# Kernel tuning notes

Measured on AMD Instinct MI355X. Metric: run time of the kernel, lower is better.

Reference implementation:

```python
import jax, jax.numpy as jnp
import numpy as np

B, N = 4096, 12
HID = 64
SLOPE = 0.2   # GATv2Conv default negative_slope
ALPHA = 0.1   # skip-connection scale


def _gabriel_adjacency(p):
    # p: [B, N, 2] node positions. Gabriel graph: edge (i,j) iff no other
    # point k lies inside the closed disk with diameter segment (p_i, p_j).
    n = p.shape[1]
    mid = (p[:, :, None, :] + p[:, None, :, :]) * 0.5                      # [B,N,N,2]
    r2 = jnp.sum((p[:, :, None, :] - p[:, None, :, :]) ** 2, -1) * 0.25    # [B,N,N]
    d2 = jnp.sum((p[:, None, None, :, :] - mid[:, :, :, None, :]) ** 2, -1)  # [B,i,j,k]
    eye = jnp.eye(n, dtype=bool)
    excl = eye[:, None, :] | eye[None, :, :]                               # k==i or k==j
    d2 = jnp.where(excl[None], jnp.inf, d2)
    gab = jnp.all(d2 > r2[..., None], axis=-1) & (~eye)[None]
    # undirected edges + self loops (GATv2Conv add_self_loops=True default)
    return gab | jnp.swapaxes(gab, 1, 2) | eye[None]                       # [B,N,N]


def _gatv2(x, adj, wl, wr, att, b):
    # PyG GATv2Conv, heads=1: e_ij = att . leaky_relu(W_l x_j + W_r x_i),
    # alpha = softmax_j(e_ij) over neighbors, out_i = sum_j alpha_ij W_l x_j + b.
    xl = x @ wl                                                            # source feats [B,N,H]
    xr = x @ wr                                                            # target feats [B,N,H]
    s = jax.nn.leaky_relu(xl[:, None, :, :] + xr[:, :, None, :], SLOPE)    # [B,i,j,H]
    e = jnp.einsum('bijh,h->bij', s, att)
    e = jnp.where(adj, e, -1e9)
    a = jax.nn.softmax(e, axis=-1)                                         # over sources j
    return jnp.einsum('bij,bjh->bih', a, xl) + b


def _forward(batch, enc_w1, enc_b1, enc_w2, enc_b2, enc_w3, enc_b3,
             g1_wl, g1_wr, g1_att, g1_b, g2_wl, g2_wr, g2_att, g2_b,
             g3_wl, g3_wr, g3_att, g3_b, g4_wl, g4_wr, g4_att, g4_b,
             lab_w, lab_b, val_w, val_b, skip_w, skip_b):
    h = jax.nn.relu(batch @ enc_w1 + enc_b1)
    h = jax.nn.relu(h @ enc_w2 + enc_b2)
    latent = h @ enc_w3 + enc_b3                                           # [B,N,3]
    # graph construction is non-differentiable (scipy in the original)
    adj = _gabriel_adjacency(jax.lax.stop_gradient(latent[..., :2]))
    x0 = latent[..., 2:3]                                                  # [B,N,1]
    x1 = jax.nn.relu(_gatv2(x0, adj, g1_wl, g1_wr, g1_att, g1_b))
    x2 = jax.nn.relu(_gatv2(x1, adj, g2_wl, g2_wr, g2_att, g2_b))
    skip = latent @ skip_w + skip_b
    x3 = jax.nn.relu(_gatv2(x2, adj, g3_wl, g3_wr, g3_att, g3_b) + ALPHA * skip)
    logits = x3 @ lab_w + lab_b                                            # [B,N,4]
    # note: original feeds x2 (not x3) into gcn4 -- kept faithful
    x4 = jax.nn.relu(_gatv2(x2, adj, g4_wl, g4_wr, g4_att, g4_b) + ALPHA * skip)
    values = x4 @ val_w + val_b                                            # [B,N,1]
    return batch[:, :, :4], batch[:, :, 4:5], logits, values, latent


def setup_inputs():
    key = jax.random.key(0)
    ks = iter(jax.random.split(key, 40))
    def rnd(shape, s=0.1):
        return jax.random.normal(next(ks), shape, dtype=jnp.float32) * s
    inp = {"batch": jax.random.normal(next(ks), (B, N, 5), dtype=jnp.float32)}
    inp.update(enc_w1=rnd((5, HID)), enc_b1=jnp.zeros((HID,), jnp.float32),
               enc_w2=rnd((HID, HID)), enc_b2=jnp.zeros((HID,), jnp.float32),
               enc_w3=rnd((HID, 3)), enc_b3=jnp.zeros((3,), jnp.float32))
    for i, cin in zip((1, 2, 3, 4), (1, HID, HID, HID)):
        inp[f"g{i}_wl"] = rnd((cin, HID)); inp[f"g{i}_wr"] = rnd((cin, HID))
        inp[f"g{i}_att"] = rnd((HID,)); inp[f"g{i}_b"] = jnp.zeros((HID,), jnp.float32)
    inp.update(lab_w=rnd((HID, 4)), lab_b=jnp.zeros((4,), jnp.float32),
               val_w=rnd((HID, 1)), val_b=jnp.zeros((1,), jnp.float32),
               skip_w=rnd((3, HID)), skip_b=jnp.zeros((HID,), jnp.float32))
    return inp


def reference(batch, enc_w1, enc_b1, enc_w2, enc_b2, enc_w3, enc_b3,
              g1_wl, g1_wr, g1_att, g1_b, g2_wl, g2_wr, g2_att, g2_b,
              g3_wl, g3_wr, g3_att, g3_b, g4_wl, g4_wr, g4_att, g4_b,
              lab_w, lab_b, val_w, val_b, skip_w, skip_b):
    return _forward(batch, enc_w1, enc_b1, enc_w2, enc_b2, enc_w3, enc_b3,
                    g1_wl, g1_wr, g1_att, g1_b, g2_wl, g2_wr, g2_att, g2_b,
                    g3_wl, g3_wr, g3_att, g3_b, g4_wl, g4_wr, g4_att, g4_b,
                    lab_w, lab_b, val_w, val_b, skip_w, skip_b)
```

## Files before the change

### kernel.cpp

```cpp
#include <hip/hip_runtime.h>
#include <hip/hip_bf16.h>
#include <math.h>

#define N     12
#define HID   64
#define STP   68
#define XST   72
#define SLOPE 0.2f
#define ALPHA 0.1f

typedef float v2f __attribute__((ext_vector_type(2)));
typedef float v4f __attribute__((ext_vector_type(4)));
typedef int   i4  __attribute__((ext_vector_type(4)));
typedef short v8s __attribute__((ext_vector_type(8)));

static __device__ __forceinline__ v8s as_v8s(i4 v) {
    union { i4 a; v8s b; } u; u.a = v; return u.b;
}
static __device__ __forceinline__ unsigned short f2bf(float f) {
    __hip_bfloat16 h = __float2bfloat16(f);
    return *(unsigned short*)&h;
}
static __device__ __forceinline__ float bf2f(unsigned short u) {
    return __uint_as_float((unsigned)u << 16);
}

#define OUT0 0
#define OUT1 196608
#define OUT2 245760
#define OUT3 442368
#define OUT4 491520

__global__ void prep_kernel(const float* __restrict__ enc_w2,
                            const float* __restrict__ g2_wl, const float* __restrict__ g2_wr,
                            const float* __restrict__ g3_wl, const float* __restrict__ g3_wr,
                            const float* __restrict__ g4_wl, const float* __restrict__ g4_wr,
                            const float* __restrict__ lab_w,
                            float* __restrict__ ws) {
    int t = threadIdx.x;
    int bx = blockIdx.x;
    if (bx < 64) { ws[t*64 + bx] = enc_w2[bx*64 + t]; return; }
    if (bx == 112) {
        #pragma unroll
        for (int c = 0; c < 4; c++) ws[16384 + c*64 + t] = lab_w[t*4 + c];
        return;
    }
    int idx = bx - 64;
    int mat = idx >> 3, rem = idx & 7;
    int kt = rem >> 2, nt = rem & 3;
    const float* src;
    switch (mat) {
        case 0: src = g2_wl; break;
        case 1: src = g2_wr; break;
        case 2: src = g3_wl; break;
        case 3: src = g3_wr; break;
        case 4: src = g4_wl; break;
        default: src = g4_wr; break;
    }
    int quad = t >> 4, col = t & 15;
    int n = nt*16 + col;
    unsigned* dst = (unsigned*)(ws + 4096) + mat*2048 + (kt*4+nt)*256 + t*4;
    #pragma unroll
    for (int jp = 0; jp < 4; jp++) {
        int k0 = kt*32 + quad*8 + 2*jp;
        dst[jp] = (unsigned)f2bf(src[(k0+0)*64 + n]) | ((unsigned)f2bf(src[(k0+1)*64 + n]) << 16);
    }
}

template<bool TW>
__global__ __launch_bounds__(64, 3) void gae_kernel(
    const float* __restrict__ batch,
    const float* __restrict__ enc_w1, const float* __restrict__ enc_b1,
    const float* __restrict__ enc_w2, const float* __restrict__ enc_b2,
    const float* __restrict__ enc_w3, const float* __restrict__ enc_b3,
    const float* __restrict__ g1_wl, const float* __restrict__ g1_wr,
    const float* __restrict__ g1_att, const float* __restrict__ g1_b,
    const float* __restrict__ g2_wl, const float* __restrict__ g2_wr,
    const float* __restrict__ g2_att, const float* __restrict__ g2_b,
    const float* __restrict__ g3_wl, const float* __restrict__ g3_wr,
    const float* __restrict__ g3_att, const float* __restrict__ g3_b,
    const float* __restrict__ g4_wl, const float* __restrict__ g4_wr,
    const float* __restrict__ g4_att, const float* __restrict__ g4_b,
    const float* __restrict__ lab_w, const float* __restrict__ lab_b,
    const float* __restrict__ val_w, const float* __restrict__ val_b,
    const float* __restrict__ skip_w, const float* __restrict__ skip_b,
    const float* __restrict__ wsT,
    float* __restrict__ out)
{
    const int b = blockIdx.x;
    const int t = threadIdx.x;

    __shared__ __align__(16) unsigned char smem[7424];
    float* h1 = (float*)smem;
    float* h2 = (float*)(smem + 3264);
    unsigned short* xl16 = (unsigned short*)smem;
    unsigned short* xr16 = (unsigned short*)(smem + 1728);
    unsigned short* xB16 = (unsigned short*)(smem + 3456);
    float* pool  = (float*)(smem + 6528);
    float* att_s = (float*)(smem + 7104);
    unsigned char* pairs8 = smem + 7360;

    const v2f z2 = {0.f, 0.f};
    const v4f z4 = {0.f, 0.f, 0.f, 0.f};
    const v2f sl2 = {SLOPE, SLOPE};

    const int p0 = t,        i0 = p0 / N, j0 = p0 - i0*N;
    const int p1 = t + 64,   i1 = p1 / N, j1 = p1 - i1*N;
    const int p2 = (t < 16) ? (t + 128) : 143;
    const int i2 = p2 / N,   j2 = p2 - i2*N;

    if (t < N*5) {
        float v = batch[b*(N*5) + t];
        int i = t / 5, f = t - i*5;
        if (f < 4) out[OUT0 + (size_t)b*(N*4) + i*4 + f] = v;
        else       out[OUT1 + (size_t)b*N + i] = v;
    }

    {
        float acc[N];
        float bias = enc_b1[t];
        #pragma unroll
        for (int i=0;i<N;i++) acc[i] = bias;
        const float* brow = batch + b*(N*5);
        #pragma unroll
        for (int f=0; f<5; f++) {
            float w = enc_w1[f*HID + t];
            #pragma unroll
            for (int i=0;i<N;i++) acc[i] = fmaf(brow[i*5+f], w, acc[i]);
        }
        #pragma unroll
        for (int i=0;i<N;i++) h1[i*STP + t] = fmaxf(acc[i], 0.f);
    }
    __syncthreads();

    {
        v2f acc[N];
        #pragma unroll
        for (int i=0;i<N;i++) acc[i] = z2;
        const float* w2p = TW ? (wsT + t*HID) : nullptr;
        for (int c=0;c<HID;c+=4) {
            v2f w01, w23;
            if (TW) {
                v4f w4 = *reinterpret_cast<const v4f*>(&w2p[c]);
                w01 = w4.xy; w23 = w4.zw;
            } else {
                w01 = (v2f){enc_w2[(c+0)*HID+t], enc_w2[(c+1)*HID+t]};
                w23 = (v2f){enc_w2[(c+2)*HID+t], enc_w2[(c+3)*HID+t]};
            }
            #pragma unroll
            for (int i=0;i<N;i++) {
                v4f xv = *reinterpret_cast<const v4f*>(&h1[i*STP + c]);
                acc[i] = __builtin_elementwise_fma(xv.xy, w01, acc[i]);
                acc[i] = __builtin_elementwise_fma(xv.zw, w23, acc[i]);
            }
        }
        float bias = enc_b2[t];
        #pragma unroll
        for (int i=0;i<N;i++) h2[i*STP + t] = fmaxf(bias + acc[i].x + acc[i].y, 0.f);
    }
    __syncthreads();

    if (t < N*3) {
        int i = t / 3, c = t - i*3;
        float acc = enc_b3[c];
        for (int k=0;k<HID;k+=4) {
            v4f xv = *reinterpret_cast<const v4f*>(&h2[i*STP + k]);
            acc = fmaf(xv.x, enc_w3[(k+0)*3+c], acc);
            acc = fmaf(xv.y, enc_w3[(k+1)*3+c], acc);
            acc = fmaf(xv.z, enc_w3[(k+2)*3+c], acc);
            acc = fmaf(xv.w, enc_w3[(k+3)*3+c], acc);
        }
        pool[t] = acc;
        out[OUT4 + (size_t)b*(N*3) + t] = acc;
    }
    __syncthreads();

    float kx[N], ky[N], kz[N];
    #pragma unroll
    for (int k=0;k<N;k++) { kx[k]=pool[k*3]; ky[k]=pool[k*3+1]; kz[k]=pool[k*3+2]; }

    float skipv[N];
    {
        float w0 = skip_w[t], w1 = skip_w[HID+t], w2 = skip_w[2*HID+t];
        float bias = skip_b[t];
        #pragma unroll
        for (int i=0;i<N;i++)
            skipv[i] = fmaf(kx[i], w0, fmaf(ky[i], w1, fmaf(kz[i], w2, bias)));
    }

    auto gab = [&](int i, int j)->bool {
        if (i == j) return false;
        float pix = pool[i*3], piy = pool[i*3+1];
        float pjx = pool[j*3], pjy = pool[j*3+1];
        float mx = (pix + pjx) * 0.5f, my = (piy + pjy) * 0.5f;
        float dx = pix - pjx, dy = piy - pjy;
        float r2 = (dx*dx + dy*dy) * 0.25f;
        bool g = true;
        #pragma unroll
        for (int k=0;k<N;k++) {
            float ex = kx[k] - mx, ey = ky[k] - my;
            bool ok = (k == i) || (k == j) || (ex*ex + ey*ey > r2);
            g = g && ok;
        }
        return g;
    };
    unsigned long long gb0 = __ballot(gab(i0, j0));
    unsigned long long gb1 = __ballot(gab(i1, j1));
    unsigned long long gb2 = __ballot((t < 16) && gab(i2, j2));
    auto gbit = [&](int p)->int {
        unsigned long long m = (p < 64) ? gb0 : ((p < 128) ? gb1 : gb2);
        return (int)((m >> (p & 63)) & 1ull);
    };
    const int adjA = gbit(p0) | gbit(j0*N+i0) | (i0 == j0);
    const int adjB = gbit(p1) | gbit(j1*N+i1) | (i1 == j1);
    const int adjC = (t < 16) ? (gbit(p2) | gbit(j2*N+i2) | (i2 == j2)) : 0;

    auto mbcnt64 = [&](unsigned long long m)->int {
        return __builtin_amdgcn_mbcnt_hi((unsigned)(m >> 32),
               __builtin_amdgcn_mbcnt_lo((unsigned)m, 0));
    };
    const unsigned long long am0 = __ballot(adjA != 0);
    const unsigned long long am1 = __ballot(adjB != 0);
    const unsigned long long am2 = __ballot(adjC != 0);
    const int c0  = __popcll(am0);
    const int c01 = c0 + __popcll(am1);
    const int nv  = c01 + __popcll(am2);
    const int idx0 = mbcnt64(am0);
    const int idx1 = c0  + mbcnt64(am1);
    const int idx2 = c01 + mbcnt64(am2);
    if (adjA)               pairs8[idx0] = (unsigned char)p0;
    if (adjB && idx1 < 64)  pairs8[idx1] = (unsigned char)p1;
    if (adjC && idx2 < 64)  pairs8[idx2] = (unsigned char)p2;
    const bool ovB = adjB && (idx1 >= 64);
    const bool ovC = adjC && (idx2 >= 64);
    const int nvc = nv < 64 ? nv : 64;

    auto scoreAt = [&](int i, int j)->float {
        const unsigned* Lj = (const unsigned*)&xl16[j*XST];
        const unsigned* Ri = (const unsigned*)&xr16[i*XST];
        v2f a2 = z2;
        for (int h=0; h<HID; h+=8) {
            i4 lw = *reinterpret_cast<const i4*>(Lj + (h>>1));
            i4 rw = *reinterpret_cast<const i4*>(Ri + (h>>1));
            v4f aa = *reinterpret_cast<const v4f*>(&att_s[h]);
            v4f ab = *reinterpret_cast<const v4f*>(&att_s[h+4]);
            #pragma unroll
            for (int q=0; q<4; q++) {
                unsigned lu = (unsigned)lw[q], ru = (unsigned)rw[q];
                v2f xl2 = { __uint_as_float(lu << 16), __uint_as_float(lu & 0xffff0000u) };
                v2f xr2 = { __uint_as_float(ru << 16), __uint_as_float(ru & 0xffff0000u) };
                v2f s = xl2 + xr2;
                v2f l = __builtin_elementwise_fma(sl2, __builtin_elementwise_min(s, z2),
                                                  __builtin_elementwise_max(s, z2));
                v2f av = (q==0) ? aa.xy : (q==1) ? aa.zw : (q==2) ? ab.xy : ab.zw;
                a2 = __builtin_elementwise_fma(av, l, a2);
            }
        }
        return a2.x + a2.y;
    };

    auto gat_core = [&](const float* __restrict__ att, const float* __restrict__ gb,
                        unsigned short* __restrict__ out16, int useSkip) {
        att_s[t] = att[t];
        pool[t] = 0.f; pool[t+64] = 0.f;
        if (t < 16) pool[t+128] = 0.f;
        __syncthreads();
        if (t < nvc) {
            int p = pairs8[t];
            int i = (p * 171) >> 11;
            int j = p - i*N;
            pool[p] = __expf(scoreAt(i, j));
        }
        if (nv > 64) {
            if (ovB) pool[p1] = __expf(scoreAt(i1, j1));
            if (ovC) pool[p2] = __expf(scoreAt(i2, j2));
        }
        __syncthreads();
        {
            float xj[N];
            #pragma unroll
            for (int j=0;j<N;j++) xj[j] = bf2f(xl16[j*XST + t]);
            v4f X0 = {xj[0], xj[1], xj[2],  xj[3]};
            v4f X1 = {xj[4], xj[5], xj[6],  xj[7]};
            v4f X2 = {xj[8], xj[9], xj[10], xj[11]};
            float bias = gb[t];
            #pragma unroll
            for (int i=0;i<N;i++) {
                const v4f* ep = reinterpret_cast<const v4f*>(&pool[i*N]);
                v4f e0 = ep[0], e1 = ep[1], e2 = ep[2];
                float sum = ((e0.x+e0.y)+(e0.z+e0.w))
                          + ((e1.x+e1.y)+(e1.z+e1.w))
                          + ((e2.x+e2.y)+(e2.z+e2.w));
                v4f acc = __builtin_elementwise_fma(e0, X0,
                          __builtin_elementwise_fma(e1, X1, e2*X2));
                float r = bias + ((acc.x + acc.y) + (acc.z + acc.w)) / sum;
                if (useSkip) r = fmaf(ALPHA, skipv[i], r);
                out16[i*XST + t] = f2bf(fmaxf(r, 0.f));
            }
        }
        __syncthreads();
    };

    auto stage_mfma = [&](int matL) {
        const int m = t & 15, quad = t >> 4;
        const int mc = (m < N) ? m : 0;
        i4 aF0 = *reinterpret_cast<const i4*>(&xB16[mc*XST + quad*8]);
        i4 aF1 = *reinterpret_cast<const i4*>(&xB16[mc*XST + 32 + quad*8]);
        const i4* bbase = reinterpret_cast<const i4*>(wsT + 4096);
        #pragma unroll
        for (int mm=0; mm<2; mm++) {
            const i4* bp = bbase + (matL + mm)*512;
            v4f acc[4] = {z4, z4, z4, z4};
            #pragma unroll
            for (int nt=0; nt<4; nt++) {
                i4 b0 = bp[(0*4+nt)*64 + t];
                i4 b1 = bp[(1*4+nt)*64 + t];
                acc[nt] = __builtin_amdgcn_mfma_f32_16x16x32_bf16(as_v8s(aF0), as_v8s(b0), acc[nt], 0, 0, 0);
                acc[nt] = __builtin_amdgcn_mfma_f32_16x16x32_bf16(as_v8s(aF1), as_v8s(b1), acc[nt], 0, 0, 0);
            }
            unsigned short* dst = (mm == 0) ? xl16 : xr16;
            if (quad < 3) {
                #pragma unroll
                for (int nt=0; nt<4; nt++) {
                    #pragma unroll
                    for (int r=0; r<4; r++)
                        dst[(quad*4+r)*XST + nt*16 + m] = f2bf(acc[nt][r]);
                }
            }
        }
    };

    auto stage = [&](const float* __restrict__ wl, const float* __restrict__ wr) {
        v2f al[N], ar[N];
        #pragma unroll
        for (int i=0;i<N;i++) { al[i] = z2; ar[i] = z2; }
        for (int c=0;c<HID;c+=2) {
            v2f wlv = (v2f){wl[(c+0)*HID+t], wl[(c+1)*HID+t]};
            v2f wrv = (v2f){wr[(c+0)*HID+t], wr[(c+1)*HID+t]};
            #pragma unroll
            for (int i=0;i<N;i++) {
                unsigned xu = *(const unsigned*)&xB16[i*XST + c];
                v2f xv = { __uint_as_float(xu << 16), __uint_as_float(xu & 0xffff0000u) };
                al[i] = __builtin_elementwise_fma(xv, wlv, al[i]);
                ar[i] = __builtin_elementwise_fma(xv, wrv, ar[i]);
            }
        }
        #pragma unroll
        for (int i=0;i<N;i++) {
            xl16[i*XST + t] = f2bf(al[i].x + al[i].y);
            xr16[i*XST + t] = f2bf(ar[i].x + ar[i].y);
        }
    };

    {
        float wlv = g1_wl[t], wrv = g1_wr[t];
        #pragma unroll
        for (int i=0;i<N;i++) {
            xl16[i*XST + t] = f2bf(kz[i] * wlv);
            xr16[i*XST + t] = f2bf(kz[i] * wrv);
        }
    }
    gat_core(g1_att, g1_b, xB16, 0);

    if (TW) stage_mfma(0); else stage(g2_wl, g2_wr);
    gat_core(g2_att, g2_b, xB16, 0);

    if (TW) stage_mfma(2); else stage(g3_wl, g3_wr);
    gat_core(g3_att, g3_b, xr16, 1);

    if (t < N*4) {
        int i = t >> 2, c = t & 3;
        float acc = lab_b[c];
        const unsigned* xp = (const unsigned*)&xr16[i*XST];
        if (TW) {
            const float* lwT = wsT + 16384 + c*HID;
            for (int h=0;h<HID;h+=2) {
                unsigned xu = xp[h>>1];
                acc = fmaf(__uint_as_float(xu << 16), lwT[h], acc);
                acc = fmaf(__uint_as_float(xu & 0xffff0000u), lwT[h+1], acc);
            }
        } else {
            for (int h=0;h<HID;h+=2) {
                unsigned xu = xp[h>>1];
                acc = fmaf(__uint_as_float(xu << 16), lab_w[(h+0)*4+c], acc);
                acc = fmaf(__uint_as_float(xu & 0xffff0000u), lab_w[(h+1)*4+c], acc);
            }
        }
        out[OUT2 + (size_t)b*(N*4) + t] = acc;
    }

    if (TW) stage_mfma(4); else stage(g4_wl, g4_wr);
    gat_core(g4_att, g4_b, xr16, 1);

    if (t < N) {
        float acc = val_b[0];
        const unsigned* xp = (const unsigned*)&xr16[t*XST];
        for (int h=0;h<HID;h+=2) {
            unsigned xu = xp[h>>1];
            acc = fmaf(__uint_as_float(xu << 16), val_w[h], acc);
            acc = fmaf(__uint_as_float(xu & 0xffff0000u), val_w[h+1], acc);
        }
        out[OUT3 + (size_t)b*N + t] = acc;
    }
}

extern "C" void kernel_launch(void* const* d_in, const int* in_sizes, int n_in,
                              void* d_out, int out_size, void* d_ws, size_t ws_size,
                              hipStream_t stream) {
    (void)in_sizes; (void)n_in; (void)out_size;
    const bool useT = (ws_size >= (16384 + 256)*sizeof(float));
    if (useT) {
        prep_kernel<<<dim3(113), dim3(64), 0, stream>>>(
            (const float*)d_in[3],
            (const float*)d_in[11], (const float*)d_in[12],
            (const float*)d_in[15], (const float*)d_in[16],
            (const float*)d_in[19], (const float*)d_in[20],
            (const float*)d_in[23],
            (float*)d_ws);
        gae_kernel<true><<<dim3(4096), dim3(64), 0, stream>>>(
            (const float*)d_in[0],
            (const float*)d_in[1],  (const float*)d_in[2],
            (const float*)d_in[3],  (const float*)d_in[4],
            (const float*)d_in[5],  (const float*)d_in[6],
            (const float*)d_in[7],  (const float*)d_in[8],  (const float*)d_in[9],  (const float*)d_in[10],
            (const float*)d_in[11], (const float*)d_in[12], (const float*)d_in[13], (const float*)d_in[14],
            (const float*)d_in[15], (const float*)d_in[16], (const float*)d_in[17], (const float*)d_in[18],
            (const float*)d_in[19], (const float*)d_in[20], (const float*)d_in[21], (const float*)d_in[22],
            (const float*)d_in[23], (const float*)d_in[24],
            (const float*)d_in[25], (const float*)d_in[26],
            (const float*)d_in[27], (const float*)d_in[28],
            (const float*)d_ws,
            (float*)d_out);
    } else {
        gae_kernel<false><<<dim3(4096), dim3(64), 0, stream>>>(
            (const float*)d_in[0],
            (const float*)d_in[1],  (const float*)d_in[2],
            (const float*)d_in[3],  (const float*)d_in[4],
            (const float*)d_in[5],  (const float*)d_in[6],
            (const float*)d_in[7],  (const float*)d_in[8],  (const float*)d_in[9],  (const float*)d_in[10],
            (const float*)d_in[11], (const float*)d_in[12], (const float*)d_in[13], (const float*)d_in[14],
            (const float*)d_in[15], (const float*)d_in[16], (const float*)d_in[17], (const float*)d_in[18],
            (const float*)d_in[19], (const float*)d_in[20], (const float*)d_in[21], (const float*)d_in[22],
            (const float*)d_in[23], (const float*)d_in[24],
            (const float*)d_in[25], (const float*)d_in[26],
            (const float*)d_in[27], (const float*)d_in[28],
            nullptr,
            (float*)d_out);
    }
}
```

Baseline: 174.5 us.

## Reduce register pressure: read pool from LDS, split shared buffers, batch Gabriel tests

Drops the per-thread kx/ky/kz register arrays and reads latent coordinates from shared memory instead. The batch row is now staged through LDS for the first encoder layer. The three Gabriel pair tests per thread are interleaved in one loop over k. Shared memory becomes separate named arrays instead of one aliased byte buffer, and an extra barrier is added before stage 4. The aim is lower VGPR use and better latency hiding, at the cost of more LDS reads, extra barriers and a larger LDS footprint.

Result: no change. 176.7 us (+1.3%).

```diff
diff --git a/kernel.cpp b/kernel.cpp
--- a/kernel.cpp
+++ b/kernel.cpp
@@ -90,15 +90,15 @@
     const int b = blockIdx.x;
     const int t = threadIdx.x;
 
-    __shared__ __align__(16) unsigned char smem[7424];
-    float* h1 = (float*)smem;
-    float* h2 = (float*)(smem + 3264);
-    unsigned short* xl16 = (unsigned short*)smem;
-    unsigned short* xr16 = (unsigned short*)(smem + 1728);
-    unsigned short* xB16 = (unsigned short*)(smem + 3456);
-    float* pool  = (float*)(smem + 6528);
-    float* att_s = (float*)(smem + 7104);
-    unsigned char* pairs8 = smem + 7360;
+    __shared__ __align__(16) float bufA[N*STP];
+    __shared__ __align__(16) float bufB[N*STP];
+    __shared__ __align__(16) unsigned short xB16[N*XST];
+    __shared__ __align__(16) float pool[144];
+    __shared__ __align__(16) float att_s[HID];
+    __shared__ __align__(16) unsigned char pairs8[64];
+
+    unsigned short* xl16 = (unsigned short*)bufA;
+    unsigned short* xr16 = (unsigned short*)bufB;
 
     const v2f z2 = {0.f, 0.f};
     const v4f z4 = {0.f, 0.f, 0.f, 0.f};
@@ -111,25 +111,26 @@
 
     if (t < N*5) {
         float v = batch[b*(N*5) + t];
+        pool[t] = v;
         int i = t / 5, f = t - i*5;
         if (f < 4) out[OUT0 + (size_t)b*(N*4) + i*4 + f] = v;
         else       out[OUT1 + (size_t)b*N + i] = v;
     }
+    __syncthreads();
 
     {
         float acc[N];
         float bias = enc_b1[t];
         #pragma unroll
         for (int i=0;i<N;i++) acc[i] = bias;
-        const float* brow = batch + b*(N*5);
         #pragma unroll
         for (int f=0; f<5; f++) {
             float w = enc_w1[f*HID + t];
             #pragma unroll
-            for (int i=0;i<N;i++) acc[i] = fmaf(brow[i*5+f], w, acc[i]);
-        }
-        #pragma unroll
-        for (int i=0;i<N;i++) h1[i*STP + t] = fmaxf(acc[i], 0.f);
+            for (int i=0;i<N;i++) acc[i] = fmaf(pool[i*5+f], w, acc[i]);
+        }
+        #pragma unroll
+        for (int i=0;i<N;i++) bufA[i*STP + t] = fmaxf(acc[i], 0.f);
     }
     __syncthreads();
 
@@ -149,14 +150,14 @@
             }
             #pragma unroll
             for (int i=0;i<N;i++) {
-                v4f xv = *reinterpret_cast<const v4f*>(&h1[i*STP + c]);
+                v4f xv = *reinterpret_cast<const v4f*>(&bufA[i*STP + c]);
                 acc[i] = __builtin_elementwise_fma(xv.xy, w01, acc[i]);
                 acc[i] = __builtin_elementwise_fma(xv.zw, w23, acc[i]);
             }
         }
         float bias = enc_b2[t];
         #pragma unroll
-        for (int i=0;i<N;i++) h2[i*STP + t] = fmaxf(bias + acc[i].x + acc[i].y, 0.f);
+        for (int i=0;i<N;i++) bufB[i*STP + t] = fmaxf(bias + acc[i].x + acc[i].y, 0.f);
     }
     __syncthreads();
 
@@ -164,7 +165,7 @@
         int i = t / 3, c = t - i*3;
         float acc = enc_b3[c];
         for (int k=0;k<HID;k+=4) {
-            v4f xv = *reinterpret_cast<const v4f*>(&h2[i*STP + k]);
+            v4f xv = *reinterpret_cast<const v4f*>(&bufB[i*STP + k]);
             acc = fmaf(xv.x, enc_w3[(k+0)*3+c], acc);
             acc = fmaf(xv.y, enc_w3[(k+1)*3+c], acc);
             acc = fmaf(xv.z, enc_w3[(k+2)*3+c], acc);
@@ -175,38 +176,52 @@
     }
     __syncthreads();
 
-    float kx[N], ky[N], kz[N];
-    #pragma unroll
-    for (int k=0;k<N;k++) { kx[k]=pool[k*3]; ky[k]=pool[k*3+1]; kz[k]=pool[k*3+2]; }
-
     float skipv[N];
     {
         float w0 = skip_w[t], w1 = skip_w[HID+t], w2 = skip_w[2*HID+t];
         float bias = skip_b[t];
         #pragma unroll
-        for (int i=0;i<N;i++)
-            skipv[i] = fmaf(kx[i], w0, fmaf(ky[i], w1, fmaf(kz[i], w2, bias)));
-    }
-
-    auto gab = [&](int i, int j)->bool {
-        if (i == j) return false;
-        float pix = pool[i*3], piy = pool[i*3+1];
-        float pjx = pool[j*3], pjy = pool[j*3+1];
-        float mx = (pix + pjx) * 0.5f, my = (piy + pjy) * 0.5f;
-        float dx = pix - pjx, dy = piy - pjy;
-        float r2 = (dx*dx + dy*dy) * 0.25f;
-        bool g = true;
+        for (int i=0;i<N;i++) {
+            float v = bias;
+            v = fmaf(pool[i*3+0], w0, v);
+            v = fmaf(pool[i*3+1], w1, v);
+            v = fmaf(pool[i*3+2], w2, v);
+            skipv[i] = v;
+        }
+    }
+
+    bool g0v, g1v, g2v;
+    {
+        float a0x = pool[i0*3], a0y = pool[i0*3+1];
+        float b0x = pool[j0*3], b0y = pool[j0*3+1];
+        float a1x = pool[i1*3], a1y = pool[i1*3+1];
+        float b1x = pool[j1*3], b1y = pool[j1*3+1];
+        float a2x = pool[i2*3], a2y = pool[i2*3+1];
+        float b2x = pool[j2*3], b2y = pool[j2*3+1];
+        float m0x = (a0x+b0x)*0.5f, m0y = (a0y+b0y)*0.5f;
+        float m1x = (a1x+b1x)*0.5f, m1y = (a1y+b1y)*0.5f;
+        float m2x = (a2x+b2x)*0.5f, m2y = (a2y+b2y)*0.5f;
+        float d0x = a0x-b0x, d0y = a0y-b0y;
+        float d1x = a1x-b1x, d1y = a1y-b1y;
+        float d2x = a2x-b2x, d2y = a2y-b2y;
+        float r20 = (d0x*d0x + d0y*d0y)*0.25f;
+        float r21 = (d1x*d1x + d1y*d1y)*0.25f;
+        float r22 = (d2x*d2x + d2y*d2y)*0.25f;
+        g0v = (i0 != j0); g1v = (i1 != j1); g2v = (t < 16) && (i2 != j2);
         #pragma unroll
         for (int k=0;k<N;k++) {
-            float ex = kx[k] - mx, ey = ky[k] - my;
-            bool ok = (k == i) || (k == j) || (ex*ex + ey*ey > r2);
-            g = g && ok;
-        }
-        return g;
-    };
-    unsigned long long gb0 = __ballot(gab(i0, j0));
-    unsigned long long gb1 = __ballot(gab(i1, j1));
-    unsigned long long gb2 = __ballot((t < 16) && gab(i2, j2));
+            float ekx = pool[k*3], eky = pool[k*3+1];
+            float e0x = ekx-m0x, e0y = eky-m0y;
+            float e1x = ekx-m1x, e1y = eky-m1y;
+            float e2x = ekx-m2x, e2y = eky-m2y;
+            g0v = g0v && ((k==i0)||(k==j0)||(e0x*e0x + e0y*e0y > r20));
+            g1v = g1v && ((k==i1)||(k==j1)||(e1x*e1x + e1y*e1y > r21));
+            g2v = g2v && ((k==i2)||(k==j2)||(e2x*e2x + e2y*e2y > r22));
+        }
+    }
+    unsigned long long gb0 = __ballot(g0v);
+    unsigned long long gb1 = __ballot(g1v);
+    unsigned long long gb2 = __ballot(g2v);
     auto gbit = [&](int p)->int {
         unsigned long long m = (p < 64) ? gb0 : ((p < 128) ? gb1 : gb2);
         return (int)((m >> (p & 63)) & 1ull);
@@ -236,14 +251,14 @@
     const int nvc = nv < 64 ? nv : 64;
 
     auto scoreAt = [&](int i, int j)->float {
-        const unsigned* Lj = (const unsigned*)&xl16[j*XST];
-        const unsigned* Ri = (const unsigned*)&xr16[i*XST];
+        const i4* Lj = reinterpret_cast<const i4*>(xl16 + j*XST);
+        const i4* Ri = reinterpret_cast<const i4*>(xr16 + i*XST);
         v2f a2 = z2;
-        for (int h=0; h<HID; h+=8) {
-            i4 lw = *reinterpret_cast<const i4*>(Lj + (h>>1));
-            i4 rw = *reinterpret_cast<const i4*>(Ri + (h>>1));
-            v4f aa = *reinterpret_cast<const v4f*>(&att_s[h]);
-            v4f ab = *reinterpret_cast<const v4f*>(&att_s[h+4]);
+        for (int h=0; h<8; h++) {
+            i4 lw = Lj[h];
+            i4 rw = Ri[h];
+            v4f aa = *reinterpret_cast<const v4f*>(&att_s[h*8]);
+            v4f ab = *reinterpret_cast<const v4f*>(&att_s[h*8+4]);
             #pragma unroll
             for (int q=0; q<4; q++) {
                 unsigned lu = (unsigned)lw[q], ru = (unsigned)rw[q];
@@ -356,8 +371,9 @@
         float wlv = g1_wl[t], wrv = g1_wr[t];
         #pragma unroll
         for (int i=0;i<N;i++) {
-            xl16[i*XST + t] = f2bf(kz[i] * wlv);
-            xr16[i*XST + t] = f2bf(kz[i] * wrv);
+            float v = pool[i*3+2];
+            xl16[i*XST + t] = f2bf(v * wlv);
+            xr16[i*XST + t] = f2bf(v * wrv);
         }
     }
     gat_core(g1_att, g1_b, xB16, 0);
@@ -388,6 +404,7 @@
         }
         out[OUT2 + (size_t)b*(N*4) + t] = acc;
     }
+    __syncthreads();
 
     if (TW) stage_mfma(4); else stage(g4_wl, g4_wr);
     gat_core(g4_att, g4_b, xr16, 1);
```
